# Kernel tuning notes

Hardware: AMD Instinct MI355X
Metric: run time of the kernel (lower is better)

Reference implementation:

```python
import jax, jax.numpy as jnp
import numpy as np

B, N, DIN, H, C, K = 2, 16384, 1024, 512, 11, 100
SCORE_THRESH = 0.05
NMS_THRESH = 0.5
WX, WY, WW, WH = 10.0, 10.0, 5.0, 5.0
BBOX_XFORM_CLIP = float(np.log(1000.0 / 16.0))


def setup_inputs() -> dict:
    key = jax.random.key(0)
    ks = jax.random.split(key, 8)
    x = jax.random.normal(ks[0], (B * N, DIN), jnp.float32)
    # proposals: valid xyxy in first 4 coords, 5 extra box params after
    xy = jax.random.uniform(ks[1], (B, N, 2), jnp.float32) * 512.0
    wh = jax.random.uniform(ks[2], (B, N, 2), jnp.float32) * 64.0 + 1.0
    rest = jax.random.normal(ks[3], (B, N, 5), jnp.float32)
    proposals = jnp.concatenate([xy, xy + wh, rest], axis=-1)  # [B,N,9]
    s = 0.02
    w1 = jax.random.normal(ks[4], (DIN, H), jnp.float32) * s
    b1 = jnp.zeros((H,), jnp.float32)
    w2 = jax.random.normal(ks[5], (H, H), jnp.float32) * s
    b2 = jnp.zeros((H,), jnp.float32)
    wc = jax.random.normal(ks[6], (H, C), jnp.float32) * s
    bc = jnp.zeros((C,), jnp.float32)
    wr = jax.random.normal(ks[7], (H, C * 9), jnp.float32) * s
    br = jnp.zeros((C * 9,), jnp.float32)
    return dict(x=x, proposals=proposals, w1=w1, b1=b1, w2=w2, b2=b2,
                wc=wc, bc=bc, wr=wr, br=br)


def decode(reg, proposals):
    # reg [B,N,C,9], proposals [B,N,9]; BoxCoder.decode with weights (10,10,5,5)
    widths = proposals[..., 2] - proposals[..., 0]
    heights = proposals[..., 3] - proposals[..., 1]
    ctr_x = proposals[..., 0] + 0.5 * widths
    ctr_y = proposals[..., 1] + 0.5 * heights
    dx = reg[..., 0] / WX
    dy = reg[..., 1] / WY
    dw = jnp.minimum(reg[..., 2] / WW, BBOX_XFORM_CLIP)
    dh = jnp.minimum(reg[..., 3] / WH, BBOX_XFORM_CLIP)
    pcx = dx * widths[..., None] + ctr_x[..., None]
    pcy = dy * heights[..., None] + ctr_y[..., None]
    pw = jnp.exp(dw) * widths[..., None]
    ph = jnp.exp(dh) * heights[..., None]
    xyxy = jnp.stack([pcx - 0.5 * pw, pcy - 0.5 * ph,
                      pcx + 0.5 * pw, pcy + 0.5 * ph], axis=-1)
    rest = proposals[..., None, 4:] + reg[..., 4:]  # passthrough extra 5 dims
    return jnp.concatenate([xyxy, rest], axis=-1)


def iou_one(box, boxes):
    # box [4], boxes [M,4] -> [M]
    x1 = jnp.maximum(box[0], boxes[:, 0])
    y1 = jnp.maximum(box[1], boxes[:, 1])
    x2 = jnp.minimum(box[2], boxes[:, 2])
    y2 = jnp.minimum(box[3], boxes[:, 3])
    inter = jnp.maximum(x2 - x1, 0.0) * jnp.maximum(y2 - y1, 0.0)
    a = (box[2] - box[0]) * (box[3] - box[1])
    b = (boxes[:, 2] - boxes[:, 0]) * (boxes[:, 3] - boxes[:, 1])
    return inter / (a + b - inter + 1e-9)


def nms_frame(obox4, scores_masked):
    # greedy NMS, fixed K iterations (keep[:detections_per_frame])
    def step(s, _):
        i = jnp.argmax(s)
        sc = s[i]
        iou = iou_one(obox4[i], obox4)
        s2 = jnp.where(iou > NMS_THRESH, -jnp.inf, s)
        s2 = s2.at[i].set(-jnp.inf)
        return s2, (i, sc > -jnp.inf)
    _, (idx, pick) = jax.lax.scan(step, scores_masked, None, length=K)
    return idx, pick


def forward_core(x, proposals, w1, b1, w2, b2, wc, bc, wr, br):
    Bn, Nn = proposals.shape[0], proposals.shape[1]
    h = jax.nn.relu(x @ w1 + b1)          # box_head mlp
    h = jax.nn.relu(h @ w2 + b2)
    logits = (h @ wc + bc).reshape(Bn, Nn, C)
    reg = (h @ wr + br).reshape(Bn, Nn, C, 9)
    boxes = decode(reg, proposals)                     # [B,N,C,9]
    scores = jax.nn.softmax(logits, axis=-1)
    # drop background class 0, flatten class dim
    boxes = boxes[:, :, 1:, :].reshape(Bn, Nn * (C - 1), 9)
    scores = scores[:, :, 1:].reshape(Bn, Nn * (C - 1))
    labels = jnp.tile(jnp.arange(1, C), Nn)            # [N*(C-1)]
    bw = boxes[..., 2] - boxes[..., 0]
    bh = boxes[..., 3] - boxes[..., 1]
    # score_thresh filter + remove_small_boxes(min_size=0.01), expressed as a mask
    valid = (scores > SCORE_THRESH) & (bw >= 0.01) & (bh >= 0.01)
    # batched_nms via per-class coordinate offset trick
    max_coord = jnp.max(jnp.abs(boxes[..., :4]))
    obox = boxes[..., :4] + (labels.astype(boxes.dtype) * (max_coord + 1.0))[None, :, None]
    s0 = jnp.where(valid, scores, -jnp.inf)

    def frame(ob, b9, s_raw, s_masked):
        idx, pick = nms_frame(ob, s_masked)
        bo = b9[idx]                                   # [K,9]
        so = jnp.where(pick, s_raw[idx], 0.0)
        lo = jnp.where(pick, labels[idx], -1)
        return bo, so, lo

    return jax.vmap(frame)(obox, boxes, scores, s0)


def reference(x, proposals, w1, b1, w2, b2, wc, bc, wr, br):
    boxes, scores, labels = forward_core(x, proposals, w1, b1, w2, b2, wc, bc, wr, br)
    return boxes, scores, labels
```

## Files before the change

### kernel.cpp

```cpp
#include <hip/hip_runtime.h>
#include <stdint.h>

#define NFRAMES 2
#define NPROP   16384
#define NROWS   (NFRAMES * NPROP)
#define DIN_    1024
#define HDIM    512
#define NCLS    11
#define LRLD    128
#define NBINS   8192
#define CAP     4096
#define TGT     1024
#define KKEEP   100
#define SCORE_T 0.05f
#define NMS_T   0.5f
#define CLIPV   4.135166556742356f
#define BK      16

#define OFF_H1      0ULL
#define OFF_H2      67108864ULL
#define OFF_LR      134217728ULL
#define OFF_WCAT    150994944ULL
#define OFF_BCAT    151257088ULL
#define OFF_SCORES  151258112ULL
#define OFF_HIST    152568832ULL
#define OFF_GCNT    152634368ULL
#define OFF_TAU     152634376ULL
#define OFF_GKEYS   152634624ULL
#define WS_NEEDED   152700160ULL

__device__ __forceinline__ void decode4(const float* __restrict__ prop,
                                        const float* __restrict__ rg,
                                        float& x1, float& y1, float& x2, float& y2) {
    float w  = prop[2] - prop[0];
    float h  = prop[3] - prop[1];
    float cx = prop[0] + 0.5f * w;
    float cy = prop[1] + 0.5f * h;
    float dx = rg[0] / 10.0f;
    float dy = rg[1] / 10.0f;
    float dw = fminf(rg[2] / 5.0f, CLIPV);
    float dh = fminf(rg[3] / 5.0f, CLIPV);
    float pcx = dx * w + cx;
    float pcy = dy * h + cy;
    float pw  = expf(dw) * w;
    float ph  = expf(dh) * h;
    x1 = pcx - 0.5f * pw;
    y1 = pcy - 0.5f * ph;
    x2 = pcx + 0.5f * pw;
    y2 = pcy + 0.5f * ph;
}

__global__ __launch_bounds__(256) void gemm128(const float* __restrict__ A,
                                               const float* __restrict__ B,
                                               const float* __restrict__ bias,
                                               float* __restrict__ C,
                                               int K, int N, int do_relu) {
    __shared__ float As[2][BK][128];
    __shared__ float Bs[2][BK][128];
    const int tid  = threadIdx.x;
    const int row0 = blockIdx.x * 128;
    const int col0 = blockIdx.y * 128;
    const int tx = tid & 15, ty = tid >> 4;

    const int arow  = tid >> 1;
    const int akoff = (tid & 1) * 8;
    const int brow  = tid >> 5;
    const int bc4   = (tid & 31) * 4;

    const float* Ap = A + (size_t)(row0 + arow) * K + akoff;
    const float* Bp = B + col0 + bc4;

    float acc[8][8];
#pragma unroll
    for (int i = 0; i < 8; ++i)
#pragma unroll
        for (int j = 0; j < 8; ++j) acc[i][j] = 0.f;

    float4 a0 = *(const float4*)(Ap + 0);
    float4 a1 = *(const float4*)(Ap + 4);
    float4 b0 = *(const float4*)(Bp + (size_t)brow * N);
    float4 b1 = *(const float4*)(Bp + (size_t)(brow + 8) * N);
    As[0][akoff + 0][arow] = a0.x;
    As[0][akoff + 1][arow] = a0.y;
    As[0][akoff + 2][arow] = a0.z;
    As[0][akoff + 3][arow] = a0.w;
    As[0][akoff + 4][arow] = a1.x;
    As[0][akoff + 5][arow] = a1.y;
    As[0][akoff + 6][arow] = a1.z;
    As[0][akoff + 7][arow] = a1.w;
    *(float4*)&Bs[0][brow][bc4]     = b0;
    *(float4*)&Bs[0][brow + 8][bc4] = b1;
    __syncthreads();

    int p = 0;
    for (int k0 = 0; k0 < K; k0 += BK) {
        const bool has_next = (k0 + BK) < K;
        if (has_next) {
            a0 = *(const float4*)(Ap + k0 + BK);
            a1 = *(const float4*)(Ap + k0 + BK + 4);
            b0 = *(const float4*)(Bp + (size_t)(k0 + BK + brow) * N);
            b1 = *(const float4*)(Bp + (size_t)(k0 + BK + brow + 8) * N);
        }
#pragma unroll
        for (int kk = 0; kk < BK; ++kk) {
            float4 x0 = *(const float4*)&As[p][kk][ty * 4];
            float4 x1 = *(const float4*)&As[p][kk][64 + ty * 4];
            float4 y0 = *(const float4*)&Bs[p][kk][tx * 4];
            float4 y1 = *(const float4*)&Bs[p][kk][64 + tx * 4];
            float ar[8] = {x0.x, x0.y, x0.z, x0.w, x1.x, x1.y, x1.z, x1.w};
            float br[8] = {y0.x, y0.y, y0.z, y0.w, y1.x, y1.y, y1.z, y1.w};
#pragma unroll
            for (int i = 0; i < 8; ++i)
#pragma unroll
                for (int j = 0; j < 8; ++j) acc[i][j] += ar[i] * br[j];
        }
        if (has_next) {
            const int q = p ^ 1;
            As[q][akoff + 0][arow] = a0.x;
            As[q][akoff + 1][arow] = a0.y;
            As[q][akoff + 2][arow] = a0.z;
            As[q][akoff + 3][arow] = a0.w;
            As[q][akoff + 4][arow] = a1.x;
            As[q][akoff + 5][arow] = a1.y;
            As[q][akoff + 6][arow] = a1.z;
            As[q][akoff + 7][arow] = a1.w;
            *(float4*)&Bs[q][brow][bc4]     = b0;
            *(float4*)&Bs[q][brow + 8][bc4] = b1;
            __syncthreads();
            p = q;
        }
    }

#pragma unroll
    for (int qi = 0; qi < 2; ++qi)
#pragma unroll
        for (int i = 0; i < 4; ++i) {
            int row = row0 + qi * 64 + ty * 4 + i;
#pragma unroll
            for (int qj = 0; qj < 2; ++qj) {
                int col = col0 + qj * 64 + tx * 4;
                float4 v;
                v.x = acc[qi * 4 + i][qj * 4 + 0] + bias[col + 0];
                v.y = acc[qi * 4 + i][qj * 4 + 1] + bias[col + 1];
                v.z = acc[qi * 4 + i][qj * 4 + 2] + bias[col + 2];
                v.w = acc[qi * 4 + i][qj * 4 + 3] + bias[col + 3];
                if (do_relu) {
                    v.x = fmaxf(v.x, 0.f); v.y = fmaxf(v.y, 0.f);
                    v.z = fmaxf(v.z, 0.f); v.w = fmaxf(v.w, 0.f);
                }
                *(float4*)(C + (size_t)row * N + col) = v;
            }
        }
}

__global__ void concat_w(const float* __restrict__ wc, const float* __restrict__ bc,
                         const float* __restrict__ wr, const float* __restrict__ br,
                         float* __restrict__ wcat, float* __restrict__ bcat) {
    int gid = blockIdx.x * 256 + threadIdx.x;
    if (gid >= HDIM * LRLD) return;
    int k = gid >> 7, j = gid & 127;
    float v = 0.f;
    if (j < 11)       v = wc[k * 11 + j];
    else if (j < 110) v = wr[k * 99 + (j - 11)];
    wcat[gid] = v;
    if (k == 0) {
        float b = 0.f;
        if (j < 11)       b = bc[j];
        else if (j < 110) b = br[j - 11];
        bcat[j] = b;
    }
}

__global__ __launch_bounds__(256) void softmax_hist(const float* __restrict__ logreg,
                                                    float* __restrict__ scores,
                                                    int* __restrict__ hist) {
    __shared__ int lh[NBINS];
    const int t = threadIdx.x;
    for (int i = t; i < NBINS; i += 256) lh[i] = 0;
    __syncthreads();

    const int r = blockIdx.x * 256 + t;
    const float* lr = logreg + (size_t)r * LRLD;
    float4 v0 = *(const float4*)(lr);
    float4 v1 = *(const float4*)(lr + 4);
    float4 v2 = *(const float4*)(lr + 8);
    float l[NCLS] = {v0.x, v0.y, v0.z, v0.w, v1.x, v1.y, v1.z, v1.w, v2.x, v2.y, v2.z};
    float m = l[0];
#pragma unroll
    for (int j = 1; j < NCLS; ++j) m = fmaxf(m, l[j]);
    float e[NCLS]; float s = 0.f;
#pragma unroll
    for (int j = 0; j < NCLS; ++j) { e[j] = expf(l[j] - m); s += e[j]; }
#pragma unroll
    for (int c = 1; c < NCLS; ++c) {
        float p = e[c] / s;
        scores[(size_t)r * 10 + (c - 1)] = p;
        if (p > SCORE_T) {
            int bin = (int)(p * (float)NBINS);
            bin = min(max(bin, 0), NBINS - 1);
            atomicAdd(&lh[bin], 1);
        }
    }
    __syncthreads();
    const int b = (blockIdx.x * 256) >> 14;
    for (int i = t; i < NBINS; i += 256) {
        int c = lh[i];
        if (c) atomicAdd(&hist[b * NBINS + i], c);
    }
}

__global__ __launch_bounds__(1024) void select_tau(const int* __restrict__ hist,
                                                   int* __restrict__ taubin) {
    __shared__ int seg[1024];
    __shared__ int best;
    const int b = blockIdx.x, t = threadIdx.x;
    if (t == 0) best = 0;
    const int base = t * 8;
    int loc[8];
    int s = 0;
#pragma unroll
    for (int i = 7; i >= 0; --i) {
        s += hist[b * NBINS + base + i];
        loc[i] = s;
    }
    seg[t] = s;
    __syncthreads();
    for (int off = 1; off < 1024; off <<= 1) {
        int v = (t + off < 1024) ? seg[t + off] : 0;
        __syncthreads();
        seg[t] += v;
        __syncthreads();
    }
    const int above = (t + 1 < 1024) ? seg[t + 1] : 0;
    int bmax = -1;
#pragma unroll
    for (int i = 0; i < 8; ++i) {
        if (loc[i] + above >= TGT) bmax = base + i;
    }
    if (bmax >= 0) atomicMax(&best, bmax);
    __syncthreads();
    if (t == 0) taubin[b] = best;
}

__global__ void gather_cand(const float* __restrict__ scores,
                            const float* __restrict__ logreg,
                            const float* __restrict__ proposals,
                            const int* __restrict__ taubin,
                            int* __restrict__ gcount,
                            unsigned long long* __restrict__ gkeys) {
    int gid = blockIdx.x * 256 + threadIdx.x;
    if (gid >= NROWS * 10) return;
    int r  = gid / 10;
    int ci = gid - r * 10;
    int b  = r >> 14;
    float p = scores[gid];
    int bin = (int)(p * (float)NBINS);
    bin = min(max(bin, 0), NBINS - 1);
    if (bin < taubin[b]) return;
    if (!(p > SCORE_T)) return;
    float x1, y1, x2, y2;
    decode4(proposals + (size_t)r * 9, logreg + (size_t)r * LRLD + 11 + (ci + 1) * 9,
            x1, y1, x2, y2);
    if (!((x2 - x1) >= 0.01f && (y2 - y1) >= 0.01f)) return;
    int pos = atomicAdd(&gcount[b], 1);
    if (pos < CAP) {
        unsigned int sb   = __float_as_uint(p);
        unsigned int cand = (unsigned)(r - b * NPROP) * 10u + (unsigned)ci;
        gkeys[(size_t)b * CAP + pos] =
            ((unsigned long long)(0xFFFFFFFFu - sb) << 32) | (unsigned long long)cand;
    }
}

__global__ __launch_bounds__(1024) void sort_cand(int* __restrict__ gcount,
                                                  unsigned long long* __restrict__ gkeys) {
    __shared__ unsigned long long sk[CAP];
    int b = blockIdx.x, tid = threadIdx.x;
    int gc = gcount[b]; if (gc > CAP) gc = CAP;
    for (int i = tid; i < CAP; i += 1024)
        sk[i] = (i < gc) ? gkeys[(size_t)b * CAP + i] : ~0ULL;
    __syncthreads();
    for (int k = 2; k <= CAP; k <<= 1) {
        for (int j = k >> 1; j > 0; j >>= 1) {
            for (int i = tid; i < CAP; i += 1024) {
                int ixj = i ^ j;
                if (ixj > i) {
                    bool up = ((i & k) == 0);
                    unsigned long long a = sk[i], c = sk[ixj];
                    if ((a > c) == up) { sk[i] = c; sk[ixj] = a; }
                }
            }
            __syncthreads();
        }
    }
    for (int i = tid; i < CAP; i += 1024)
        gkeys[(size_t)b * CAP + i] = sk[i];
    if (tid == 0 && gcount[b] > CAP) gcount[b] = CAP;
}

#define NPRE 2048
__global__ __launch_bounds__(64) void nms_out(const unsigned long long* __restrict__ gkeys,
                                              const int* __restrict__ gcount,
                                              const float* __restrict__ scores,
                                              const float* __restrict__ logreg,
                                              const float* __restrict__ proposals,
                                              float* __restrict__ out) {
    int b = blockIdx.x, tid = threadIdx.x;
    __shared__ unsigned long long skeys[NPRE];
    __shared__ float kbox[KKEEP][4];
    __shared__ int   kcls[KKEEP];
    __shared__ int   kcand[KKEEP];
    __shared__ int   kcount;
    if (tid == 0) kcount = 0;
    int gc = min(gcount[b], CAP);
    for (int i = tid; i < NPRE; i += 64)
        if (i < gc) skeys[i] = gkeys[(size_t)b * CAP + i];
    __syncthreads();
    for (int ptr = 0; ptr < gc; ++ptr) {
        __syncthreads();
        int kc = kcount;
        if (kc >= KKEEP) break;
        unsigned long long key = (ptr < NPRE) ? skeys[ptr] : gkeys[(size_t)b * CAP + ptr];
        unsigned int cand = (unsigned int)(key & 0xFFFFFFFFULL);
        int n = cand / 10;
        int c = (int)(cand - n * 10) + 1;
        int r = b * NPROP + n;
        float x1, y1, x2, y2;
        decode4(proposals + (size_t)r * 9, logreg + (size_t)r * LRLD + 11 + c * 9,
                x1, y1, x2, y2);
        int sup = 0;
        for (int q = tid; q < kc; q += 64) {
            if (kcls[q] == c) {
                float xx1 = fmaxf(x1, kbox[q][0]);
                float yy1 = fmaxf(y1, kbox[q][1]);
                float xx2 = fminf(x2, kbox[q][2]);
                float yy2 = fminf(y2, kbox[q][3]);
                float inter = fmaxf(xx2 - xx1, 0.f) * fmaxf(yy2 - yy1, 0.f);
                float aa = (kbox[q][2] - kbox[q][0]) * (kbox[q][3] - kbox[q][1]);
                float ab = (x2 - x1) * (y2 - y1);
                float iou = inter / (aa + ab - inter + 1e-9f);
                if (iou > NMS_T) sup = 1;
            }
        }
        if (!__any(sup)) {
            if (tid == 0) {
                kbox[kc][0] = x1; kbox[kc][1] = y1; kbox[kc][2] = x2; kbox[kc][3] = y2;
                kcls[kc] = c; kcand[kc] = (int)cand; kcount = kc + 1;
            }
        }
    }
    __syncthreads();
    int kc = min(kcount, KKEEP);
    for (int k = tid; k < KKEEP; k += 64) {
        int cand = (k < kc) ? kcand[k] : 0;
        int n = cand / 10;
        int c = cand - n * 10 + 1;
        int r = b * NPROP + n;
        const float* prop = proposals + (size_t)r * 9;
        const float* rg = logreg + (size_t)r * LRLD + 11 + c * 9;
        float x1, y1, x2, y2;
        decode4(prop, rg, x1, y1, x2, y2);
        float* ob = out + ((size_t)b * KKEEP + k) * 9;
        ob[0] = x1; ob[1] = y1; ob[2] = x2; ob[3] = y2;
#pragma unroll
        for (int j = 0; j < 5; ++j) ob[4 + j] = prop[4 + j] + rg[4 + j];
        out[NFRAMES * KKEEP * 9 + b * KKEEP + k] =
            (k < kc) ? scores[(size_t)r * 10 + (c - 1)] : 0.f;
        out[NFRAMES * KKEEP * 9 + NFRAMES * KKEEP + b * KKEEP + k] =
            (k < kc) ? (float)c : -1.0f;
    }
}

extern "C" void kernel_launch(void* const* d_in, const int* in_sizes, int n_in,
                              void* d_out, int out_size, void* d_ws, size_t ws_size,
                              hipStream_t stream) {
    (void)in_sizes; (void)n_in; (void)out_size;
    if (ws_size < WS_NEEDED) return;

    const float* x         = (const float*)d_in[0];
    const float* proposals = (const float*)d_in[1];
    const float* w1        = (const float*)d_in[2];
    const float* b1        = (const float*)d_in[3];
    const float* w2        = (const float*)d_in[4];
    const float* b2        = (const float*)d_in[5];
    const float* wc        = (const float*)d_in[6];
    const float* bc        = (const float*)d_in[7];
    const float* wr        = (const float*)d_in[8];
    const float* br        = (const float*)d_in[9];
    float* out = (float*)d_out;

    char* ws = (char*)d_ws;
    float* h1     = (float*)(ws + OFF_H1);
    float* h2     = (float*)(ws + OFF_H2);
    float* logreg = (float*)(ws + OFF_LR);
    float* wcat   = (float*)(ws + OFF_WCAT);
    float* bcat   = (float*)(ws + OFF_BCAT);
    float* scores = (float*)(ws + OFF_SCORES);
    int*   hist   = (int*)(ws + OFF_HIST);
    int*   gcount = (int*)(ws + OFF_GCNT);
    int*   taubin = (int*)(ws + OFF_TAU);
    unsigned long long* gkeys = (unsigned long long*)(ws + OFF_GKEYS);

    hipMemsetAsync(hist, 0, (size_t)(NFRAMES * NBINS * 4 + 256), stream);

    concat_w<<<(HDIM * LRLD + 255) / 256, 256, 0, stream>>>(wc, bc, wr, br, wcat, bcat);

    gemm128<<<dim3(NROWS / 128, HDIM / 128), 256, 0, stream>>>(x,  w1,   b1,   h1,     DIN_, HDIM, 1);
    gemm128<<<dim3(NROWS / 128, HDIM / 128), 256, 0, stream>>>(h1, w2,   b2,   h2,     HDIM, HDIM, 1);
    gemm128<<<dim3(NROWS / 128, 1),          256, 0, stream>>>(h2, wcat, bcat, logreg, HDIM, LRLD, 0);

    softmax_hist<<<NROWS / 256, 256, 0, stream>>>(logreg, scores, hist);
    select_tau<<<NFRAMES, 1024, 0, stream>>>(hist, taubin);
    gather_cand<<<(NROWS * 10 + 255) / 256, 256, 0, stream>>>(scores, logreg, proposals,
                                                              taubin, gcount, gkeys);
    sort_cand<<<NFRAMES, 1024, 0, stream>>>(gcount, gkeys);
    nms_out<<<NFRAMES, 64, 0, stream>>>(gkeys, gcount, scores, logreg, proposals, out);
}
```

Before: 997.9 us.

## Use 128x256 FP32 GEMM tiles with direct global-to-LDS loads; shrink sort size

Adds a templated GEMM kernel for the two hidden layers. It uses 128x256 output tiles with 8x16 accumulators per thread and loads global memory straight into LDS through global_load_lds, with an XOR swizzle on the A tile. The larger register tile raises arithmetic intensity, and the direct LDS loads skip the register staging path, but the larger register footprint limits occupancy to one block per CU. Separately, the bitonic candidate sort now pads only to the next power of two above the actual count (at least 1024) rather than the full capacity, which cuts sort stages when few candidates pass.

```diff
diff --git a/kernel.cpp b/kernel.cpp
--- a/kernel.cpp
+++ b/kernel.cpp
@@ -28,6 +28,15 @@
 #define OFF_TAU     152634376ULL
 #define OFF_GKEYS   152634624ULL
 #define WS_NEEDED   152700160ULL
+
+#define GLD16(gp, lp)                                                         \
+    __builtin_amdgcn_global_load_lds(                                         \
+        (const __attribute__((address_space(1))) void*)(gp),                  \
+        (__attribute__((address_space(3))) void*)(lp), 16, 0, 0)
+
+__device__ __forceinline__ float f4c(const float4& v, int i) {
+    return i == 0 ? v.x : (i == 1 ? v.y : (i == 2 ? v.z : v.w));
+}
 
 __device__ __forceinline__ void decode4(const float* __restrict__ prop,
                                         const float* __restrict__ rg,
@@ -48,6 +57,105 @@
     y1 = pcy - 0.5f * ph;
     x2 = pcx + 0.5f * pw;
     y2 = pcy + 0.5f * ph;
+}
+
+template<int K, int N, int DO_RELU>
+__global__ __launch_bounds__(256, 1) void gemm256g(const float* __restrict__ A,
+                                                   const float* __restrict__ B,
+                                                   const float* __restrict__ bias,
+                                                   float* __restrict__ C) {
+    __shared__ float As[2][128][BK];
+    __shared__ float Bs[2][BK][256];
+    const int tid  = threadIdx.x;
+    const int w    = tid >> 6;
+    const int lane = tid & 63;
+    const int row0 = blockIdx.x * 128;
+    const int col0 = blockIdx.y * 256;
+    const int tx = tid & 15, ty = tid >> 4;
+
+    const int a_row = w * 32 + (lane >> 2);
+    const int a_kc  = ((lane & 3) ^ ((lane >> 4) & 3)) * 4;
+    const int b_k   = w * 4;
+
+    const float* Asrc0 = A + (size_t)(row0 + a_row) * K + a_kc;
+    const float* Asrc1 = A + (size_t)(row0 + a_row + 16) * K + a_kc;
+    const float* Bsrc  = B + col0 + (lane << 2);
+
+#define STAGE(buf, kb)                                                        \
+    do {                                                                      \
+        GLD16(Asrc0 + (kb), &As[buf][w * 32][0]);                             \
+        GLD16(Asrc1 + (kb), &As[buf][w * 32 + 16][0]);                        \
+        GLD16(Bsrc + (size_t)((kb) + b_k + 0) * N, &Bs[buf][b_k + 0][0]);     \
+        GLD16(Bsrc + (size_t)((kb) + b_k + 1) * N, &Bs[buf][b_k + 1][0]);     \
+        GLD16(Bsrc + (size_t)((kb) + b_k + 2) * N, &Bs[buf][b_k + 2][0]);     \
+        GLD16(Bsrc + (size_t)((kb) + b_k + 3) * N, &Bs[buf][b_k + 3][0]);     \
+    } while (0)
+
+    float acc[8][16];
+#pragma unroll
+    for (int i = 0; i < 8; ++i)
+#pragma unroll
+        for (int j = 0; j < 16; ++j) acc[i][j] = 0.f;
+
+    STAGE(0, 0);
+    __syncthreads();
+
+    const int cswz = ty & 3;
+    int p = 0;
+    for (int k0 = 0; k0 < K; k0 += BK) {
+        const bool has_next = (k0 + BK) < K;
+        if (has_next) STAGE(p ^ 1, k0 + BK);
+#pragma unroll
+        for (int kq = 0; kq < 4; ++kq) {
+            float4 av[8];
+            const int pc = (kq ^ cswz) * 4;
+#pragma unroll
+            for (int qi = 0; qi < 2; ++qi)
+#pragma unroll
+                for (int i = 0; i < 4; ++i)
+                    av[qi * 4 + i] = *(const float4*)&As[p][qi * 64 + ty * 4 + i][pc];
+#pragma unroll
+            for (int t = 0; t < 4; ++t) {
+                const int kk = kq * 4 + t;
+                float4 y0 = *(const float4*)&Bs[p][kk][tx * 4];
+                float4 y1 = *(const float4*)&Bs[p][kk][64 + tx * 4];
+                float4 y2 = *(const float4*)&Bs[p][kk][128 + tx * 4];
+                float4 y3 = *(const float4*)&Bs[p][kk][192 + tx * 4];
+                const float br[16] = {y0.x, y0.y, y0.z, y0.w, y1.x, y1.y, y1.z, y1.w,
+                                      y2.x, y2.y, y2.z, y2.w, y3.x, y3.y, y3.z, y3.w};
+#pragma unroll
+                for (int i = 0; i < 8; ++i) {
+                    const float ar = f4c(av[i], t);
+#pragma unroll
+                    for (int j = 0; j < 16; ++j) acc[i][j] += ar * br[j];
+                }
+            }
+        }
+        __syncthreads();
+        if (has_next) p ^= 1;
+    }
+#undef STAGE
+
+#pragma unroll
+    for (int qi = 0; qi < 2; ++qi)
+#pragma unroll
+        for (int i = 0; i < 4; ++i) {
+            int row = row0 + qi * 64 + ty * 4 + i;
+#pragma unroll
+            for (int qj = 0; qj < 4; ++qj) {
+                int col = col0 + qj * 64 + tx * 4;
+                float4 v;
+                v.x = acc[qi * 4 + i][qj * 4 + 0] + bias[col + 0];
+                v.y = acc[qi * 4 + i][qj * 4 + 1] + bias[col + 1];
+                v.z = acc[qi * 4 + i][qj * 4 + 2] + bias[col + 2];
+                v.w = acc[qi * 4 + i][qj * 4 + 3] + bias[col + 3];
+                if (DO_RELU) {
+                    v.x = fmaxf(v.x, 0.f); v.y = fmaxf(v.y, 0.f);
+                    v.z = fmaxf(v.z, 0.f); v.w = fmaxf(v.w, 0.f);
+                }
+                *(float4*)(C + (size_t)row * N + col) = v;
+            }
+        }
 }
 
 __global__ __launch_bounds__(256) void gemm128(const float* __restrict__ A,
@@ -276,12 +384,14 @@
     __shared__ unsigned long long sk[CAP];
     int b = blockIdx.x, tid = threadIdx.x;
     int gc = gcount[b]; if (gc > CAP) gc = CAP;
-    for (int i = tid; i < CAP; i += 1024)
+    int S = 1024;
+    while (S < gc) S <<= 1;
+    for (int i = tid; i < S; i += 1024)
         sk[i] = (i < gc) ? gkeys[(size_t)b * CAP + i] : ~0ULL;
     __syncthreads();
-    for (int k = 2; k <= CAP; k <<= 1) {
+    for (int k = 2; k <= S; k <<= 1) {
         for (int j = k >> 1; j > 0; j >>= 1) {
-            for (int i = tid; i < CAP; i += 1024) {
+            for (int i = tid; i < S; i += 1024) {
                 int ixj = i ^ j;
                 if (ixj > i) {
                     bool up = ((i & k) == 0);
@@ -292,7 +402,7 @@
             __syncthreads();
         }
     }
-    for (int i = tid; i < CAP; i += 1024)
+    for (int i = tid; i < S; i += 1024)
         gkeys[(size_t)b * CAP + i] = sk[i];
     if (tid == 0 && gcount[b] > CAP) gcount[b] = CAP;
 }
@@ -404,9 +514,9 @@
 
     concat_w<<<(HDIM * LRLD + 255) / 256, 256, 0, stream>>>(wc, bc, wr, br, wcat, bcat);
 
-    gemm128<<<dim3(NROWS / 128, HDIM / 128), 256, 0, stream>>>(x,  w1,   b1,   h1,     DIN_, HDIM, 1);
-    gemm128<<<dim3(NROWS / 128, HDIM / 128), 256, 0, stream>>>(h1, w2,   b2,   h2,     HDIM, HDIM, 1);
-    gemm128<<<dim3(NROWS / 128, 1),          256, 0, stream>>>(h2, wcat, bcat, logreg, HDIM, LRLD, 0);
+    gemm256g<DIN_, HDIM, 1><<<dim3(NROWS / 128, HDIM / 256), 256, 0, stream>>>(x,  w1, b1, h1);
+    gemm256g<HDIM, HDIM, 1><<<dim3(NROWS / 128, HDIM / 256), 256, 0, stream>>>(h1, w2, b2, h2);
+    gemm128<<<dim3(NROWS / 128, 1), 256, 0, stream>>>(h2, wcat, bcat, logreg, HDIM, LRLD, 0);
 
     softmax_hist<<<NROWS / 256, 256, 0, stream>>>(logreg, scores, hist);
     select_tau<<<NFRAMES, 1024, 0, stream>>>(hist, taubin);
```

New measurement: 1.256 ms. +25.8%, slower.

## Load GEMM B tiles via global_load_lds, templatize dims, shrink bitonic sort size

Applied to the files above, without the earlier changes.

The GEMM B-operand tile now goes from global memory straight into LDS through the global_load_lds builtin instead of being staged in registers, and K, N and ReLU become template parameters so the compiler can specialise strides and the epilogue. The candidate sort now uses the smallest power of two at least 1024 that covers the actual candidate count, instead of always sorting the full 4096-entry capacity. Risks: no explicit wait on the direct-to-LDS loads before the barrier could create a race, and the LDS addressing assumes a per-wave contiguous layout.

```diff
diff --git a/kernel.cpp b/kernel.cpp
--- a/kernel.cpp
+++ b/kernel.cpp
@@ -28,6 +28,15 @@
 #define OFF_TAU     152634376ULL
 #define OFF_GKEYS   152634624ULL
 #define WS_NEEDED   152700160ULL
+
+#define GLD16(gp, lp)                                                         \
+    __builtin_amdgcn_global_load_lds(                                         \
+        (const __attribute__((address_space(1))) void*)(gp),                  \
+        (__attribute__((address_space(3))) void*)(lp), 16, 0, 0)
+
+__device__ __forceinline__ float f4c(const float4& v, int i) {
+    return i == 0 ? v.x : (i == 1 ? v.y : (i == 2 ? v.z : v.w));
+}
 
 __device__ __forceinline__ void decode4(const float* __restrict__ prop,
                                         const float* __restrict__ rg,
@@ -50,25 +59,26 @@
     y2 = pcy + 0.5f * ph;
 }
 
-__global__ __launch_bounds__(256) void gemm128(const float* __restrict__ A,
-                                               const float* __restrict__ B,
-                                               const float* __restrict__ bias,
-                                               float* __restrict__ C,
-                                               int K, int N, int do_relu) {
+template<int K, int N, int DO_RELU>
+__global__ __launch_bounds__(256) void gemm128d(const float* __restrict__ A,
+                                                const float* __restrict__ B,
+                                                const float* __restrict__ bias,
+                                                float* __restrict__ C) {
     __shared__ float As[2][BK][128];
     __shared__ float Bs[2][BK][128];
     const int tid  = threadIdx.x;
+    const int w    = tid >> 6;
+    const int lane = tid & 63;
     const int row0 = blockIdx.x * 128;
     const int col0 = blockIdx.y * 128;
     const int tx = tid & 15, ty = tid >> 4;
 
     const int arow  = tid >> 1;
     const int akoff = (tid & 1) * 8;
-    const int brow  = tid >> 5;
-    const int bc4   = (tid & 31) * 4;
-
     const float* Ap = A + (size_t)(row0 + arow) * K + akoff;
-    const float* Bp = B + col0 + bc4;
+
+    const int brow0 = w * 4 + (lane >> 5);
+    const float* Bp = B + col0 + ((lane & 31) << 2);
 
     float acc[8][8];
 #pragma unroll
@@ -78,8 +88,8 @@
 
     float4 a0 = *(const float4*)(Ap + 0);
     float4 a1 = *(const float4*)(Ap + 4);
-    float4 b0 = *(const float4*)(Bp + (size_t)brow * N);
-    float4 b1 = *(const float4*)(Bp + (size_t)(brow + 8) * N);
+    GLD16(Bp + (size_t)(brow0 + 0) * N, &Bs[0][w * 4 + 0][0]);
+    GLD16(Bp + (size_t)(brow0 + 2) * N, &Bs[0][w * 4 + 2][0]);
     As[0][akoff + 0][arow] = a0.x;
     As[0][akoff + 1][arow] = a0.y;
     As[0][akoff + 2][arow] = a0.z;
@@ -88,8 +98,6 @@
     As[0][akoff + 5][arow] = a1.y;
     As[0][akoff + 6][arow] = a1.z;
     As[0][akoff + 7][arow] = a1.w;
-    *(float4*)&Bs[0][brow][bc4]     = b0;
-    *(float4*)&Bs[0][brow + 8][bc4] = b1;
     __syncthreads();
 
     int p = 0;
@@ -98,8 +106,9 @@
         if (has_next) {
             a0 = *(const float4*)(Ap + k0 + BK);
             a1 = *(const float4*)(Ap + k0 + BK + 4);
-            b0 = *(const float4*)(Bp + (size_t)(k0 + BK + brow) * N);
-            b1 = *(const float4*)(Bp + (size_t)(k0 + BK + brow + 8) * N);
+            const int q = p ^ 1;
+            GLD16(Bp + (size_t)(k0 + BK + brow0 + 0) * N, &Bs[q][w * 4 + 0][0]);
+            GLD16(Bp + (size_t)(k0 + BK + brow0 + 2) * N, &Bs[q][w * 4 + 2][0]);
         }
 #pragma unroll
         for (int kk = 0; kk < BK; ++kk) {
@@ -107,12 +116,15 @@
             float4 x1 = *(const float4*)&As[p][kk][64 + ty * 4];
             float4 y0 = *(const float4*)&Bs[p][kk][tx * 4];
             float4 y1 = *(const float4*)&Bs[p][kk][64 + tx * 4];
-            float ar[8] = {x0.x, x0.y, x0.z, x0.w, x1.x, x1.y, x1.z, x1.w};
-            float br[8] = {y0.x, y0.y, y0.z, y0.w, y1.x, y1.y, y1.z, y1.w};
-#pragma unroll
-            for (int i = 0; i < 8; ++i)
-#pragma unroll
-                for (int j = 0; j < 8; ++j) acc[i][j] += ar[i] * br[j];
+#pragma unroll
+            for (int i = 0; i < 8; ++i) {
+                const float ar = (i < 4) ? f4c(x0, i & 3) : f4c(x1, i & 3);
+#pragma unroll
+                for (int j = 0; j < 8; ++j) {
+                    const float br = (j < 4) ? f4c(y0, j & 3) : f4c(y1, j & 3);
+                    acc[i][j] += ar * br;
+                }
+            }
         }
         if (has_next) {
             const int q = p ^ 1;
@@ -124,8 +136,6 @@
             As[q][akoff + 5][arow] = a1.y;
             As[q][akoff + 6][arow] = a1.z;
             As[q][akoff + 7][arow] = a1.w;
-            *(float4*)&Bs[q][brow][bc4]     = b0;
-            *(float4*)&Bs[q][brow + 8][bc4] = b1;
             __syncthreads();
             p = q;
         }
@@ -144,7 +154,7 @@
                 v.y = acc[qi * 4 + i][qj * 4 + 1] + bias[col + 1];
                 v.z = acc[qi * 4 + i][qj * 4 + 2] + bias[col + 2];
                 v.w = acc[qi * 4 + i][qj * 4 + 3] + bias[col + 3];
-                if (do_relu) {
+                if (DO_RELU) {
                     v.x = fmaxf(v.x, 0.f); v.y = fmaxf(v.y, 0.f);
                     v.z = fmaxf(v.z, 0.f); v.w = fmaxf(v.w, 0.f);
                 }
@@ -276,12 +286,14 @@
     __shared__ unsigned long long sk[CAP];
     int b = blockIdx.x, tid = threadIdx.x;
     int gc = gcount[b]; if (gc > CAP) gc = CAP;
-    for (int i = tid; i < CAP; i += 1024)
+    int S = 1024;
+    while (S < gc) S <<= 1;
+    for (int i = tid; i < S; i += 1024)
         sk[i] = (i < gc) ? gkeys[(size_t)b * CAP + i] : ~0ULL;
     __syncthreads();
-    for (int k = 2; k <= CAP; k <<= 1) {
+    for (int k = 2; k <= S; k <<= 1) {
         for (int j = k >> 1; j > 0; j >>= 1) {
-            for (int i = tid; i < CAP; i += 1024) {
+            for (int i = tid; i < S; i += 1024) {
                 int ixj = i ^ j;
                 if (ixj > i) {
                     bool up = ((i & k) == 0);
@@ -292,7 +304,7 @@
             __syncthreads();
         }
     }
-    for (int i = tid; i < CAP; i += 1024)
+    for (int i = tid; i < S; i += 1024)
         gkeys[(size_t)b * CAP + i] = sk[i];
     if (tid == 0 && gcount[b] > CAP) gcount[b] = CAP;
 }
@@ -404,9 +416,9 @@
 
     concat_w<<<(HDIM * LRLD + 255) / 256, 256, 0, stream>>>(wc, bc, wr, br, wcat, bcat);
 
-    gemm128<<<dim3(NROWS / 128, HDIM / 128), 256, 0, stream>>>(x,  w1,   b1,   h1,     DIN_, HDIM, 1);
-    gemm128<<<dim3(NROWS / 128, HDIM / 128), 256, 0, stream>>>(h1, w2,   b2,   h2,     HDIM, HDIM, 1);
-    gemm128<<<dim3(NROWS / 128, 1),          256, 0, stream>>>(h2, wcat, bcat, logreg, HDIM, LRLD, 0);
+    gemm128d<DIN_, HDIM, 1><<<dim3(NROWS / 128, HDIM / 128), 256, 0, stream>>>(x,  w1, b1, h1);
+    gemm128d<HDIM, HDIM, 1><<<dim3(NROWS / 128, HDIM / 128), 256, 0, stream>>>(h1, w2, b2, h2);
+    gemm128d<HDIM, LRLD, 0><<<dim3(NROWS / 128, 1),          256, 0, stream>>>(h2, wcat, bcat, logreg);
 
     softmax_hist<<<NROWS / 256, 256, 0, stream>>>(logreg, scores, hist);
     select_tau<<<NFRAMES, 1024, 0, stream>>>(hist, taubin);
```

After: 1.034 ms. 3.6% more time.
